# Kernel optimization log

Measured on AMD Instinct MI355X. Metric: run time of the kernel, lower is better.

Reference implementation:

```python
import jax, jax.numpy as jnp
import numpy as np

# GraphConvolutionSparse forward:
#   x = sparse_dropout(X)            (dropout=0.0 -> identity, kept faithful)
#   h = X @ W                        (sparse-dense matmul via segment_sum)
#   h = A @ h                        (sparse-dense matmul via segment_sum)
#   out = relu(h)

DROPOUT = 0.0  # layer default; keep_prob = 1 - dropout

def setup_inputs() -> dict:
    key = jax.random.key(0)
    k1, k2, k3, k4, k5, k6, k7 = jax.random.split(key, 7)
    N = 100000       # nodes
    D_IN = 512       # input feature dim
    D_OUT = 128      # output feature dim
    NNZ_X = 800000   # nonzeros in sparse feature matrix
    N_E = 1600000    # adjacency nonzeros (edges)
    x_vals = jax.random.normal(k1, (NNZ_X,), dtype=jnp.float32)
    x_rows = jax.random.randint(k2, (NNZ_X,), 0, N, dtype=jnp.int32)
    x_cols = jax.random.randint(k3, (NNZ_X,), 0, D_IN, dtype=jnp.int32)
    adj_vals = jax.random.uniform(k4, (N_E,), dtype=jnp.float32)
    adj_rows = jax.random.randint(k5, (N_E,), 0, N, dtype=jnp.int32)
    adj_cols = jax.random.randint(k6, (N_E,), 0, N, dtype=jnp.int32)
    init_range = np.sqrt(6.0 / (D_IN + D_OUT)).astype(np.float32)
    W = jax.random.uniform(k7, (D_IN, D_OUT), minval=-init_range, maxval=init_range, dtype=jnp.float32)
    return {"x_vals": x_vals, "x_rows": x_rows, "x_cols": x_cols,
            "adj_vals": adj_vals, "adj_rows": adj_rows, "adj_cols": adj_cols,
            "W": W, "n_nodes": N}

def reference(x_vals, x_rows, x_cols, adj_vals, adj_rows, adj_cols, W, n_nodes):
    keep_prob = 1.0 - DROPOUT
    # sparse dropout: with dropout=0.0 the mask keeps all entries and scale is 1,
    # so it reduces to the deterministic identity (faithful to tf semantics).
    vals = x_vals * (1.0 / keep_prob)
    # h = X @ W : gather weight rows by feature column, scale, scatter-add by node row
    xw = jax.ops.segment_sum(vals[:, None] * W[x_cols], x_rows, num_segments=n_nodes)  # [N, D_OUT]
    # out = A @ h : gather source-node rows, scale by edge weight, scatter-add to dest
    agg = jax.ops.segment_sum(adj_vals[:, None] * xw[adj_cols], adj_rows, num_segments=n_nodes)  # [N, D_OUT]
    return jax.nn.relu(agg)
```

## Files before the change

### kernel.cpp

```cpp
#include <hip/hip_runtime.h>
#include <hip/hip_fp16.h>


#define DOUT 128
#define RB 32
#define RB_BITS 5
#define NBMAX 4096
#define CAPL 1024
#define COLMASK 131071
#define CTH 128
#define CWAVES 2
#define CAPX 448
#define CAPA 768

static inline size_t align_up(size_t x, size_t a) { return (x + a - 1) & ~(a - 1); }

__device__ inline int2 nt_load_int2(const int2* p) {
    long long v = __builtin_nontemporal_load((const long long*)p);
    int2 r; r.x = (int)(unsigned int)(v & 0xffffffffLL); r.y = (int)(v >> 32);
    return r;
}
__device__ inline void nt_store_float2(float2* p, float2 v) {
    union { float2 f; long long l; } u; u.f = v;
    __builtin_nontemporal_store(u.l, (long long*)p);
}

__device__ inline int wave_incl_scan(int v, int lane) {
    #pragma unroll
    for (int off = 1; off < 64; off <<= 1) {
        int up = __shfl_up(v, off, 64);
        if (lane >= off) v += up;
    }
    return v;
}

__global__ __launch_bounds__(256) void prep_kernel(int* __restrict__ cnts, int ncnt,
                                                   const float* __restrict__ W,
                                                   __half2* __restrict__ Wh, int whtot) {
    int i = blockIdx.x * 256 + threadIdx.x;
    if (i < ncnt) cnts[i] = 0;
    if (i < whtot) {
        int c = i >> 6, l = i & 63;
        Wh[i] = __floats2half2_rn(W[(c << 7) + 2 * l], W[(c << 7) + 2 * l + 1]);
    }
}

__global__ __launch_bounds__(256) void hist_coarse(const int* __restrict__ xr, int nx,
                                                   const int* __restrict__ ar, int na,
                                                   int* __restrict__ cx, int* __restrict__ ca) {
    __shared__ int h[2 * NBMAX];
    for (int i = threadIdx.x; i < 2 * NBMAX; i += 256) h[i] = 0;
    __syncthreads();
    int base = blockIdx.x * 4096;
    int tot = nx + na;
    #pragma unroll
    for (int k = 0; k < 16; ++k) {
        int i = base + k * 256 + threadIdx.x;
        if (i < tot) {
            if (i < nx) atomicAdd(&h[xr[i] >> RB_BITS], 1);
            else        atomicAdd(&h[NBMAX + (ar[i - nx] >> RB_BITS)], 1);
        }
    }
    __syncthreads();
    for (int i = threadIdx.x; i < 2 * NBMAX; i += 256) {
        int c = h[i];
        if (c) {
            if (i < NBMAX) atomicAdd(&cx[i], c);
            else           atomicAdd(&ca[i - NBMAX], c);
        }
    }
}

__global__ __launch_bounds__(1024) void scan_nb(const int* __restrict__ cx, const int* __restrict__ ca,
                                                int* __restrict__ bx, int* __restrict__ ba,
                                                int* __restrict__ curx, int* __restrict__ cura, int nb) {
    const int* c = blockIdx.x ? ca : cx;
    int* bs  = blockIdx.x ? ba : bx;
    int* cur = blockIdx.x ? cura : curx;
    __shared__ int wsum[16];
    __shared__ int woff[16];
    __shared__ int carry_s, chunk_tot;
    int tid = threadIdx.x, lane = tid & 63, wid = tid >> 6;
    if (tid == 0) carry_s = 0;
    __syncthreads();
    for (int base = 0; base < nb; base += 1024) {
        int i = base + tid;
        int v = (i < nb) ? c[i] : 0;
        int incl = wave_incl_scan(v, lane);
        if (lane == 63) wsum[wid] = incl;
        __syncthreads();
        if (wid == 0 && lane < 16) {
            int s = wsum[lane];
            int is = s;
            #pragma unroll
            for (int off = 1; off < 16; off <<= 1) {
                int up = __shfl_up(is, off, 64);
                if (lane >= off) is += up;
            }
            woff[lane] = is - s;
            if (lane == 15) chunk_tot = is;
        }
        __syncthreads();
        int excl = incl - v + woff[wid] + carry_s;
        if (i < nb) { bs[i] = excl; cur[i] = excl; }
        __syncthreads();
        if (tid == 0) carry_s += chunk_tot;
        __syncthreads();
    }
    if (tid == 0) bs[nb] = carry_s;
}

__global__ __launch_bounds__(512) void bucket_scatter2(const int* __restrict__ xr, const int* __restrict__ xc,
                                                       const float* __restrict__ xv, int nx,
                                                       const int* __restrict__ ar, const int* __restrict__ ac,
                                                       const float* __restrict__ av, int na,
                                                       int* __restrict__ curx, int* __restrict__ cura,
                                                       int2* __restrict__ stx, int2* __restrict__ sta,
                                                       int nb, int nblk_x, int capx, int capa) {
    const int* rows; const int* cols; const float* vals; int n;
    int* gcur; int2* stage; int base; int cap;
    if (blockIdx.x < nblk_x) {
        rows = xr; cols = xc; vals = xv; n = nx; gcur = curx; stage = stx;
        base = blockIdx.x * 4096; cap = capx;
    } else {
        rows = ar; cols = ac; vals = av; n = na; gcur = cura; stage = sta;
        base = (blockIdx.x - nblk_x) * 4096; cap = capa;
    }
    __shared__ int h[NBMAX];
    __shared__ int bcur[NBMAX];
    for (int i = threadIdx.x; i < nb; i += 512) h[i] = 0;
    __syncthreads();
    int rr[8]; int cc[8]; float vv[8];
    #pragma unroll
    for (int k = 0; k < 8; ++k) {
        int i = base + k * 512 + threadIdx.x;
        rr[k] = -1;
        if (i < n) {
            rr[k] = __builtin_nontemporal_load(&rows[i]);
            cc[k] = __builtin_nontemporal_load(&cols[i]);
            vv[k] = __builtin_nontemporal_load(&vals[i]);
            atomicAdd(&h[rr[k] >> RB_BITS], 1);
        }
    }
    __syncthreads();
    for (int b = threadIdx.x; b < nb; b += 512) {
        int c = h[b];
        if (c) {
            int r = atomicAdd(&gcur[b], c);
            bcur[b] = (cap > 0) ? (b * cap + r) : r;
        }
    }
    __syncthreads();
    #pragma unroll
    for (int k = 0; k < 8; ++k) {
        if (rr[k] >= 0) {
            int b = rr[k] >> RB_BITS;
            int p = atomicAdd(&bcur[b], 1);
            if (cap == 0 || p < b * cap + cap)
                stage[p] = make_int2(((rr[k] & (RB - 1)) << 17) | cc[k], __float_as_int(vv[k]));
        }
    }
}


__global__ __launch_bounds__(CTH) void consumer_xw(const int* __restrict__ bx, const int* __restrict__ gcnt,
                                                   const int2* __restrict__ stage,
                                                   const __half2* __restrict__ Wh, __half2* __restrict__ xwh,
                                                   int N, int cap) {
    __shared__ int2 sp[CAPL];
    __shared__ int hoff[RB + 1];
    __shared__ int curs[RB];
    int b = blockIdx.x;
    int s, cnt;
    if (cap > 0) { s = b * cap; cnt = min(gcnt[b], cap); }
    else         { s = bx[b]; cnt = bx[b + 1] - s; }
    int tid = threadIdx.x, lane = tid & 63, wid = tid >> 6;
    bool fast = (cnt <= CAPL);
    if (tid < RB) curs[tid] = 0;
    __syncthreads();
    int2 pr[8];
    if (fast) {
        #pragma unroll
        for (int k = 0; k < 8; ++k) {
            int i = k * CTH + tid;
            if (i < cnt) {
                pr[k] = nt_load_int2(&stage[s + i]);
                atomicAdd(&curs[(pr[k].x >> 17) & (RB - 1)], 1);
            }
        }
    }
    __syncthreads();
    if (wid == 0) {
        int v = (lane < RB) ? curs[lane] : 0;
        int incl = wave_incl_scan(v, lane);
        if (lane < RB) {
            int excl = incl - v;
            hoff[lane] = excl;
            curs[lane] = excl;
            if (lane == RB - 1) hoff[RB] = incl;
        }
    }
    __syncthreads();
    if (fast) {
        #pragma unroll
        for (int k = 0; k < 8; ++k) {
            int i = k * CTH + tid;
            if (i < cnt) {
                int r = (pr[k].x >> 17) & (RB - 1);
                sp[atomicAdd(&curs[r], 1)] = pr[k];
            }
        }
    }
    __syncthreads();
    int row0 = b << RB_BITS;
    #pragma unroll 1
    for (int rr = 0; rr < RB / CWAVES; ++rr) {
        int r = wid + rr * CWAVES;
        int grow = row0 + r;
        if (grow >= N) continue;
        float ax = 0.f, ay = 0.f;
        if (fast) {
            int j = hoff[r], o1 = hoff[r + 1];
            for (; j + 3 < o1; j += 4) {
                int2 c0 = sp[j], c1 = sp[j + 1], c2 = sp[j + 2], c3 = sp[j + 3];
                float2 w0 = __half22float2(Wh[((size_t)(c0.x & COLMASK) << 6) + lane]);
                float2 w1 = __half22float2(Wh[((size_t)(c1.x & COLMASK) << 6) + lane]);
                float2 w2 = __half22float2(Wh[((size_t)(c2.x & COLMASK) << 6) + lane]);
                float2 w3 = __half22float2(Wh[((size_t)(c3.x & COLMASK) << 6) + lane]);
                float v0 = __int_as_float(c0.y), v1 = __int_as_float(c1.y);
                float v2 = __int_as_float(c2.y), v3 = __int_as_float(c3.y);
                ax += v0 * w0.x + v1 * w1.x + v2 * w2.x + v3 * w3.x;
                ay += v0 * w0.y + v1 * w1.y + v2 * w2.y + v3 * w3.y;
            }
            for (; j < o1; ++j) {
                int2 c0 = sp[j];
                float2 w0 = __half22float2(Wh[((size_t)(c0.x & COLMASK) << 6) + lane]);
                float v0 = __int_as_float(c0.y);
                ax += v0 * w0.x; ay += v0 * w0.y;
            }
        } else {
            for (int j = 0; j < cnt; ++j) {
                int2 c0 = stage[s + j];
                if (((c0.x >> 17) & (RB - 1)) == r) {
                    float2 w0 = __half22float2(Wh[((size_t)(c0.x & COLMASK) << 6) + lane]);
                    float v0 = __int_as_float(c0.y);
                    ax += v0 * w0.x; ay += v0 * w0.y;
                }
            }
        }
        xwh[((size_t)grow << 6) + lane] = __float22half2_rn(make_float2(ax, ay));
    }
}

__global__ __launch_bounds__(CTH) void consumer_adj(const int* __restrict__ ba, const int* __restrict__ gcnt,
                                                    const int2* __restrict__ stage,
                                                    const __half2* __restrict__ xwh, float* __restrict__ out,
                                                    int N, int cap) {
    __shared__ int2 sp[CAPL];
    __shared__ int hoff[RB + 1];
    __shared__ int curs[RB];
    int b = blockIdx.x;
    int s, cnt;
    if (cap > 0) { s = b * cap; cnt = min(gcnt[b], cap); }
    else         { s = ba[b]; cnt = ba[b + 1] - s; }
    int tid = threadIdx.x, lane = tid & 63, wid = tid >> 6;
    bool fast = (cnt <= CAPL);
    if (tid < RB) curs[tid] = 0;
    __syncthreads();
    int2 pr[8];
    if (fast) {
        #pragma unroll
        for (int k = 0; k < 8; ++k) {
            int i = k * CTH + tid;
            if (i < cnt) {
                pr[k] = nt_load_int2(&stage[s + i]);
                atomicAdd(&curs[(pr[k].x >> 17) & (RB - 1)], 1);
            }
        }
    }
    __syncthreads();
    if (wid == 0) {
        int v = (lane < RB) ? curs[lane] : 0;
        int incl = wave_incl_scan(v, lane);
        if (lane < RB) {
            int excl = incl - v;
            hoff[lane] = excl;
            curs[lane] = excl;
            if (lane == RB - 1) hoff[RB] = incl;
        }
    }
    __syncthreads();
    if (fast) {
        #pragma unroll
        for (int k = 0; k < 8; ++k) {
            int i = k * CTH + tid;
            if (i < cnt) {
                int r = (pr[k].x >> 17) & (RB - 1);
                sp[atomicAdd(&curs[r], 1)] = pr[k];
            }
        }
    }
    __syncthreads();
    int row0 = b << RB_BITS;
    #pragma unroll 1
    for (int rr = 0; rr < RB / CWAVES; ++rr) {
        int r = wid + rr * CWAVES;
        int grow = row0 + r;
        if (grow >= N) continue;
        float ax = 0.f, ay = 0.f;
        if (fast) {
            int j = hoff[r], o1 = hoff[r + 1];
            for (; j + 3 < o1; j += 4) {
                int2 c0 = sp[j], c1 = sp[j + 1], c2 = sp[j + 2], c3 = sp[j + 3];
                float2 h0 = __half22float2(xwh[((size_t)(c0.x & COLMASK) << 6) + lane]);
                float2 h1 = __half22float2(xwh[((size_t)(c1.x & COLMASK) << 6) + lane]);
                float2 h2 = __half22float2(xwh[((size_t)(c2.x & COLMASK) << 6) + lane]);
                float2 h3 = __half22float2(xwh[((size_t)(c3.x & COLMASK) << 6) + lane]);
                float v0 = __int_as_float(c0.y), v1 = __int_as_float(c1.y);
                float v2 = __int_as_float(c2.y), v3 = __int_as_float(c3.y);
                ax += v0 * h0.x + v1 * h1.x + v2 * h2.x + v3 * h3.x;
                ay += v0 * h0.y + v1 * h1.y + v2 * h2.y + v3 * h3.y;
            }
            for (; j < o1; ++j) {
                int2 c0 = sp[j];
                float2 h0 = __half22float2(xwh[((size_t)(c0.x & COLMASK) << 6) + lane]);
                float v0 = __int_as_float(c0.y);
                ax += v0 * h0.x; ay += v0 * h0.y;
            }
        } else {
            for (int j = 0; j < cnt; ++j) {
                int2 c0 = stage[s + j];
                if (((c0.x >> 17) & (RB - 1)) == r) {
                    float2 h0 = __half22float2(xwh[((size_t)(c0.x & COLMASK) << 6) + lane]);
                    float v0 = __int_as_float(c0.y);
                    ax += v0 * h0.x; ay += v0 * h0.y;
                }
            }
        }
        nt_store_float2(&((float2*)(out + (size_t)grow * DOUT))[lane],
                        make_float2(fmaxf(ax, 0.f), fmaxf(ay, 0.f)));
    }
}

__global__ void spmm_xw_atomic(const float* __restrict__ x_vals, const int* __restrict__ x_rows,
                               const int* __restrict__ x_cols, const float* __restrict__ W,
                               float* __restrict__ xw, int nnz) {
    long long t = (long long)blockIdx.x * blockDim.x + threadIdx.x;
    int i = (int)(t >> 7), d = (int)(t & 127);
    if (i >= nnz) return;
    atomicAdd(&xw[(long long)x_rows[i] * DOUT + d], x_vals[i] * W[(long long)x_cols[i] * DOUT + d]);
}
__global__ void spmm_adj_atomic(const float* __restrict__ adj_vals, const int* __restrict__ adj_rows,
                                const int* __restrict__ adj_cols, const float* __restrict__ xw,
                                float* __restrict__ out, int n_e) {
    long long t = (long long)blockIdx.x * blockDim.x + threadIdx.x;
    int e = (int)(t >> 7), d = (int)(t & 127);
    if (e >= n_e) return;
    atomicAdd(&out[(long long)adj_rows[e] * DOUT + d], adj_vals[e] * xw[(long long)adj_cols[e] * DOUT + d]);
}
__global__ void relu_kernel(float4* __restrict__ out, int n4) {
    int i = blockIdx.x * blockDim.x + threadIdx.x;
    if (i >= n4) return;
    float4 v = out[i];
    v.x = fmaxf(v.x, 0.f); v.y = fmaxf(v.y, 0.f);
    v.z = fmaxf(v.z, 0.f); v.w = fmaxf(v.w, 0.f);
    out[i] = v;
}

extern "C" void kernel_launch(void* const* d_in, const int* in_sizes, int n_in,
                              void* d_out, int out_size, void* d_ws, size_t ws_size,
                              hipStream_t stream) {
    const float* x_vals   = (const float*)d_in[0];
    const int*   x_rows   = (const int*)d_in[1];
    const int*   x_cols   = (const int*)d_in[2];
    const float* adj_vals = (const float*)d_in[3];
    const int*   adj_rows = (const int*)d_in[4];
    const int*   adj_cols = (const int*)d_in[5];
    const float* W        = (const float*)d_in[6];
    float* out = (float*)d_out;

    const int nnz_x = in_sizes[0];
    const int n_e   = in_sizes[3];
    const int N     = out_size / DOUT;
    const int D_IN  = in_sizes[6] / DOUT;
    const int nb    = (N + RB - 1) / RB;

    char* ws = (char*)d_ws;
    size_t off = 0;
    size_t xw_off   = off; off = align_up(off + (size_t)N * DOUT * sizeof(__half), 128);
    size_t wh_off   = off; off = align_up(off + (size_t)D_IN * 64 * sizeof(__half2), 128);
    size_t cx_off   = off; off += (size_t)NBMAX * sizeof(int);
    size_t ca_off   = off; off = align_up(off + (size_t)NBMAX * sizeof(int), 128);
    size_t bx_off   = off; off = align_up(off + (size_t)(NBMAX + 1) * sizeof(int), 128);
    size_t baoff    = off; off = align_up(off + (size_t)(NBMAX + 1) * sizeof(int), 128);
    size_t head = off;
    size_t sxc_off = head;
    size_t sac_off = align_up(sxc_off + (size_t)nb * CAPX * sizeof(int2), 128);
    size_t needed_cap = align_up(sac_off + (size_t)nb * CAPA * sizeof(int2), 128);
    size_t sxm_off = head;
    size_t sam_off = align_up(sxm_off + (size_t)nnz_x * sizeof(int2), 128);
    size_t needed_mid = align_up(sam_off + (size_t)n_e * sizeof(int2), 128);

    bool ok_dims = (nb <= NBMAX) && (N <= (COLMASK + 1));
    const int ncnt = 2 * NBMAX;
    const int whtot = D_IN * 64;
    const int prep_n = (ncnt > whtot ? ncnt : whtot);

    if (ok_dims && ws_size >= needed_cap) {
        __half2* xwh  = (__half2*)(ws + xw_off);
        __half2* Wh   = (__half2*)(ws + wh_off);
        int*  cx      = (int*)(ws + cx_off);
        int*  ca      = (int*)(ws + ca_off);
        int2* stage_x = (int2*)(ws + sxc_off);
        int2* stage_a = (int2*)(ws + sac_off);

        prep_kernel<<<(prep_n + 255) / 256, 256, 0, stream>>>(cx, ncnt, W, Wh, whtot);

        int nblk_x = (nnz_x + 4095) / 4096;
        int nblk_a = (n_e + 4095) / 4096;
        bucket_scatter2<<<nblk_x + nblk_a, 512, 0, stream>>>(x_rows, x_cols, x_vals, nnz_x,
                                                             adj_rows, adj_cols, adj_vals, n_e,
                                                             cx, ca, stage_x, stage_a,
                                                             nb, nblk_x, CAPX, CAPA);
        consumer_xw<<<nb, CTH, 0, stream>>>(nullptr, cx, stage_x, Wh, xwh, N, CAPX);
        consumer_adj<<<nb, CTH, 0, stream>>>(nullptr, ca, stage_a, xwh, out, N, CAPA);
    } else if (ok_dims && ws_size >= needed_mid) {
        __half2* xwh  = (__half2*)(ws + xw_off);
        __half2* Wh   = (__half2*)(ws + wh_off);
        int*  cx      = (int*)(ws + cx_off);
        int*  ca      = (int*)(ws + ca_off);
        int*  bx      = (int*)(ws + bx_off);
        int*  ba      = (int*)(ws + baoff);
        int2* stage_x = (int2*)(ws + sxm_off);
        int2* stage_a = (int2*)(ws + sam_off);

        prep_kernel<<<(prep_n + 255) / 256, 256, 0, stream>>>(cx, ncnt, W, Wh, whtot);

        int tot = nnz_x + n_e;
        hist_coarse<<<(tot + 4095) / 4096, 256, 0, stream>>>(x_rows, nnz_x, adj_rows, n_e, cx, ca);
        scan_nb<<<2, 1024, 0, stream>>>(cx, ca, bx, ba, cx, ca, nb);

        int nblk_x = (nnz_x + 4095) / 4096;
        int nblk_a = (n_e + 4095) / 4096;
        bucket_scatter2<<<nblk_x + nblk_a, 512, 0, stream>>>(x_rows, x_cols, x_vals, nnz_x,
                                                             adj_rows, adj_cols, adj_vals, n_e,
                                                             cx, ca, stage_x, stage_a,
                                                             nb, nblk_x, 0, 0);
        consumer_xw<<<nb, CTH, 0, stream>>>(bx, nullptr, stage_x, Wh, xwh, N, 0);
        consumer_adj<<<nb, CTH, 0, stream>>>(ba, nullptr, stage_a, xwh, out, N, 0);
    } else {
        float* xw = (float*)ws;
        hipMemsetAsync(xw, 0, (size_t)out_size * sizeof(float), stream);
        hipMemsetAsync(out, 0, (size_t)out_size * sizeof(float), stream);
        long long t1 = (long long)nnz_x * DOUT;
        spmm_xw_atomic<<<(int)((t1 + 255) / 256), 256, 0, stream>>>(x_vals, x_rows, x_cols, W, xw, nnz_x);
        long long t2 = (long long)n_e * DOUT;
        spmm_adj_atomic<<<(int)((t2 + 255) / 256), 256, 0, stream>>>(adj_vals, adj_rows, adj_cols, xw, out, n_e);
        relu_kernel<<<(out_size / 4 + 255) / 256, 256, 0, stream>>>((float4*)out, out_size / 4);
    }
}
```

Measured before the change: 220.5 us.

## Restructure adjacency consumer to sort edges by column chunk with LDS accumulators

The adjacency consumer now runs 256 threads (4 waves), with each wave owning 8 destination rows. Inside a bucket, edges are counting-sorted by a key that combines a source-column chunk with the row. Each wave walks the chunks in order and accumulates into a per-row float2 array in shared memory, then applies ReLU and stores. The goal is more waves per bucket and more local gathers from the half-precision xw table, at the cost of a shared-memory read-modify-write per edge and a 256-entry scan. Separately, the bucket scatter kernel now handles 8192 elements per block (16 per thread) instead of 4096, halving the block count and the global cursor atomics.

```diff
diff --git a/kernel.cpp b/kernel.cpp
--- a/kernel.cpp
+++ b/kernel.cpp
@@ -5,13 +5,18 @@
 #define DOUT 128
 #define RB 32
 #define RB_BITS 5
+#define NCH 8
+#define KMAXK 256
 #define NBMAX 4096
-#define CAPL 1024
+#define CAPLX 1024
 #define COLMASK 131071
-#define CTH 128
-#define CWAVES 2
+#define CTHX 128
+#define CWX 2
+#define CTHA 256
+#define CWA 4
 #define CAPX 448
 #define CAPA 768
+#define SCB 8192
 
 static inline size_t align_up(size_t x, size_t a) { return (x + a - 1) & ~(a - 1); }
 
@@ -121,18 +126,18 @@
     int* gcur; int2* stage; int base; int cap;
     if (blockIdx.x < nblk_x) {
         rows = xr; cols = xc; vals = xv; n = nx; gcur = curx; stage = stx;
-        base = blockIdx.x * 4096; cap = capx;
+        base = blockIdx.x * SCB; cap = capx;
     } else {
         rows = ar; cols = ac; vals = av; n = na; gcur = cura; stage = sta;
-        base = (blockIdx.x - nblk_x) * 4096; cap = capa;
+        base = (blockIdx.x - nblk_x) * SCB; cap = capa;
     }
     __shared__ int h[NBMAX];
     __shared__ int bcur[NBMAX];
     for (int i = threadIdx.x; i < nb; i += 512) h[i] = 0;
     __syncthreads();
-    int rr[8]; int cc[8]; float vv[8];
+    int rr[16]; int cc[16]; float vv[16];
     #pragma unroll
-    for (int k = 0; k < 8; ++k) {
+    for (int k = 0; k < 16; ++k) {
         int i = base + k * 512 + threadIdx.x;
         rr[k] = -1;
         if (i < n) {
@@ -152,7 +157,7 @@
     }
     __syncthreads();
     #pragma unroll
-    for (int k = 0; k < 8; ++k) {
+    for (int k = 0; k < 16; ++k) {
         if (rr[k] >= 0) {
             int b = rr[k] >> RB_BITS;
             int p = atomicAdd(&bcur[b], 1);
@@ -163,11 +168,11 @@
 }
 
 
-__global__ __launch_bounds__(CTH) void consumer_xw(const int* __restrict__ bx, const int* __restrict__ gcnt,
-                                                   const int2* __restrict__ stage,
-                                                   const __half2* __restrict__ Wh, __half2* __restrict__ xwh,
-                                                   int N, int cap) {
-    __shared__ int2 sp[CAPL];
+__global__ __launch_bounds__(CTHX) void consumer_xw(const int* __restrict__ bx, const int* __restrict__ gcnt,
+                                                    const int2* __restrict__ stage,
+                                                    const __half2* __restrict__ Wh, __half2* __restrict__ xwh,
+                                                    int N, int cap) {
+    __shared__ int2 sp[CAPLX];
     __shared__ int hoff[RB + 1];
     __shared__ int curs[RB];
     int b = blockIdx.x;
@@ -175,14 +180,14 @@
     if (cap > 0) { s = b * cap; cnt = min(gcnt[b], cap); }
     else         { s = bx[b]; cnt = bx[b + 1] - s; }
     int tid = threadIdx.x, lane = tid & 63, wid = tid >> 6;
-    bool fast = (cnt <= CAPL);
+    bool fast = (cnt <= CAPLX);
     if (tid < RB) curs[tid] = 0;
     __syncthreads();
     int2 pr[8];
     if (fast) {
         #pragma unroll
         for (int k = 0; k < 8; ++k) {
-            int i = k * CTH + tid;
+            int i = k * CTHX + tid;
             if (i < cnt) {
                 pr[k] = nt_load_int2(&stage[s + i]);
                 atomicAdd(&curs[(pr[k].x >> 17) & (RB - 1)], 1);
@@ -204,7 +209,7 @@
     if (fast) {
         #pragma unroll
         for (int k = 0; k < 8; ++k) {
-            int i = k * CTH + tid;
+            int i = k * CTHX + tid;
             if (i < cnt) {
                 int r = (pr[k].x >> 17) & (RB - 1);
                 sp[atomicAdd(&curs[r], 1)] = pr[k];
@@ -214,8 +219,8 @@
     __syncthreads();
     int row0 = b << RB_BITS;
     #pragma unroll 1
-    for (int rr = 0; rr < RB / CWAVES; ++rr) {
-        int r = wid + rr * CWAVES;
+    for (int rr = 0; rr < RB / CWX; ++rr) {
+        int r = wid + rr * CWX;
         int grow = row0 + r;
         if (grow >= N) continue;
         float ax = 0.f, ay = 0.f;
@@ -252,82 +257,112 @@
     }
 }
 
-__global__ __launch_bounds__(CTH) void consumer_adj(const int* __restrict__ ba, const int* __restrict__ gcnt,
-                                                    const int2* __restrict__ stage,
-                                                    const __half2* __restrict__ xwh, float* __restrict__ out,
-                                                    int N, int cap) {
-    __shared__ int2 sp[CAPL];
-    __shared__ int hoff[RB + 1];
-    __shared__ int curs[RB];
+
+__global__ __launch_bounds__(CTHA) void consumer_adj(const int* __restrict__ ba, const int* __restrict__ gcnt,
+                                                     const int2* __restrict__ stage,
+                                                     const __half2* __restrict__ xwh, float* __restrict__ out,
+                                                     int N, int cap) {
+    __shared__ int2 sp[CAPA];
+    __shared__ float2 accL[RB][64];
+    __shared__ int off[KMAXK + 1];
+    __shared__ int curs[KMAXK];
     int b = blockIdx.x;
     int s, cnt;
     if (cap > 0) { s = b * cap; cnt = min(gcnt[b], cap); }
     else         { s = ba[b]; cnt = ba[b + 1] - s; }
     int tid = threadIdx.x, lane = tid & 63, wid = tid >> 6;
-    bool fast = (cnt <= CAPL);
-    if (tid < RB) curs[tid] = 0;
-    __syncthreads();
-    int2 pr[8];
+    bool fast = (cnt <= CAPA);
+    curs[tid] = 0;
+    {
+        float2* af = &accL[0][0];
+        #pragma unroll
+        for (int k = 0; k < 8; ++k) af[tid + k * CTHA] = make_float2(0.f, 0.f);
+    }
+    __syncthreads();
+    int2 pr[3];
     if (fast) {
         #pragma unroll
-        for (int k = 0; k < 8; ++k) {
-            int i = k * CTH + tid;
+        for (int k = 0; k < 3; ++k) {
+            int i = k * CTHA + tid;
             if (i < cnt) {
                 pr[k] = nt_load_int2(&stage[s + i]);
-                atomicAdd(&curs[(pr[k].x >> 17) & (RB - 1)], 1);
+                int key = (((pr[k].x >> 14) & (NCH - 1)) << RB_BITS) | ((pr[k].x >> 17) & (RB - 1));
+                atomicAdd(&curs[key], 1);
             }
         }
     }
     __syncthreads();
     if (wid == 0) {
-        int v = (lane < RB) ? curs[lane] : 0;
-        int incl = wave_incl_scan(v, lane);
-        if (lane < RB) {
-            int excl = incl - v;
-            hoff[lane] = excl;
-            curs[lane] = excl;
-            if (lane == RB - 1) hoff[RB] = incl;
-        }
+        int carry = 0;
+        #pragma unroll
+        for (int q = 0; q < 4; ++q) {
+            int k = (q << 6) + lane;
+            int v = curs[k];
+            int incl = wave_incl_scan(v, lane) + carry;
+            off[k] = incl - v;
+            curs[k] = incl - v;
+            carry = __shfl(incl, 63, 64);
+        }
+        if (lane == 0) off[KMAXK] = carry;
     }
     __syncthreads();
     if (fast) {
         #pragma unroll
-        for (int k = 0; k < 8; ++k) {
-            int i = k * CTH + tid;
+        for (int k = 0; k < 3; ++k) {
+            int i = k * CTHA + tid;
             if (i < cnt) {
-                int r = (pr[k].x >> 17) & (RB - 1);
-                sp[atomicAdd(&curs[r], 1)] = pr[k];
+                int key = (((pr[k].x >> 14) & (NCH - 1)) << RB_BITS) | ((pr[k].x >> 17) & (RB - 1));
+                sp[atomicAdd(&curs[key], 1)] = pr[k];
             }
         }
     }
     __syncthreads();
     int row0 = b << RB_BITS;
-    #pragma unroll 1
-    for (int rr = 0; rr < RB / CWAVES; ++rr) {
-        int r = wid + rr * CWAVES;
-        int grow = row0 + r;
-        if (grow >= N) continue;
-        float ax = 0.f, ay = 0.f;
-        if (fast) {
-            int j = hoff[r], o1 = hoff[r + 1];
+    if (fast) {
+        int aw = wid << 3;
+        #pragma unroll 1
+        for (int ch = 0; ch < NCH; ++ch) {
+            int j  = off[(ch << RB_BITS) + aw];
+            int o1 = off[(ch << RB_BITS) + aw + 8];
             for (; j + 3 < o1; j += 4) {
                 int2 c0 = sp[j], c1 = sp[j + 1], c2 = sp[j + 2], c3 = sp[j + 3];
                 float2 h0 = __half22float2(xwh[((size_t)(c0.x & COLMASK) << 6) + lane]);
                 float2 h1 = __half22float2(xwh[((size_t)(c1.x & COLMASK) << 6) + lane]);
                 float2 h2 = __half22float2(xwh[((size_t)(c2.x & COLMASK) << 6) + lane]);
                 float2 h3 = __half22float2(xwh[((size_t)(c3.x & COLMASK) << 6) + lane]);
+                int r0 = (c0.x >> 17) & (RB - 1), r1 = (c1.x >> 17) & (RB - 1);
+                int r2 = (c2.x >> 17) & (RB - 1), r3 = (c3.x >> 17) & (RB - 1);
                 float v0 = __int_as_float(c0.y), v1 = __int_as_float(c1.y);
                 float v2 = __int_as_float(c2.y), v3 = __int_as_float(c3.y);
-                ax += v0 * h0.x + v1 * h1.x + v2 * h2.x + v3 * h3.x;
-                ay += v0 * h0.y + v1 * h1.y + v2 * h2.y + v3 * h3.y;
+                float2 a0 = accL[r0][lane]; a0.x += v0 * h0.x; a0.y += v0 * h0.y; accL[r0][lane] = a0;
+                float2 a1 = accL[r1][lane]; a1.x += v1 * h1.x; a1.y += v1 * h1.y; accL[r1][lane] = a1;
+                float2 a2 = accL[r2][lane]; a2.x += v2 * h2.x; a2.y += v2 * h2.y; accL[r2][lane] = a2;
+                float2 a3 = accL[r3][lane]; a3.x += v3 * h3.x; a3.y += v3 * h3.y; accL[r3][lane] = a3;
             }
             for (; j < o1; ++j) {
                 int2 c0 = sp[j];
                 float2 h0 = __half22float2(xwh[((size_t)(c0.x & COLMASK) << 6) + lane]);
+                int r0 = (c0.x >> 17) & (RB - 1);
                 float v0 = __int_as_float(c0.y);
-                ax += v0 * h0.x; ay += v0 * h0.y;
-            }
-        } else {
+                float2 a0 = accL[r0][lane]; a0.x += v0 * h0.x; a0.y += v0 * h0.y; accL[r0][lane] = a0;
+            }
+        }
+        #pragma unroll
+        for (int q = 0; q < 8; ++q) {
+            int grow = row0 + aw + q;
+            if (grow < N) {
+                float2 a = accL[aw + q][lane];
+                nt_store_float2(&((float2*)(out + (size_t)grow * DOUT))[lane],
+                                make_float2(fmaxf(a.x, 0.f), fmaxf(a.y, 0.f)));
+            }
+        }
+    } else {
+        #pragma unroll 1
+        for (int rr = 0; rr < RB / CWA; ++rr) {
+            int r = wid + rr * CWA;
+            int grow = row0 + r;
+            if (grow >= N) continue;
+            float ax = 0.f, ay = 0.f;
             for (int j = 0; j < cnt; ++j) {
                 int2 c0 = stage[s + j];
                 if (((c0.x >> 17) & (RB - 1)) == r) {
@@ -336,9 +371,9 @@
                     ax += v0 * h0.x; ay += v0 * h0.y;
                 }
             }
-        }
-        nt_store_float2(&((float2*)(out + (size_t)grow * DOUT))[lane],
-                        make_float2(fmaxf(ax, 0.f), fmaxf(ay, 0.f)));
+            nt_store_float2(&((float2*)(out + (size_t)grow * DOUT))[lane],
+                            make_float2(fmaxf(ax, 0.f), fmaxf(ay, 0.f)));
+        }
     }
 }
 
@@ -416,14 +451,14 @@
 
         prep_kernel<<<(prep_n + 255) / 256, 256, 0, stream>>>(cx, ncnt, W, Wh, whtot);
 
-        int nblk_x = (nnz_x + 4095) / 4096;
-        int nblk_a = (n_e + 4095) / 4096;
+        int nblk_x = (nnz_x + SCB - 1) / SCB;
+        int nblk_a = (n_e + SCB - 1) / SCB;
         bucket_scatter2<<<nblk_x + nblk_a, 512, 0, stream>>>(x_rows, x_cols, x_vals, nnz_x,
                                                              adj_rows, adj_cols, adj_vals, n_e,
                                                              cx, ca, stage_x, stage_a,
                                                              nb, nblk_x, CAPX, CAPA);
-        consumer_xw<<<nb, CTH, 0, stream>>>(nullptr, cx, stage_x, Wh, xwh, N, CAPX);
-        consumer_adj<<<nb, CTH, 0, stream>>>(nullptr, ca, stage_a, xwh, out, N, CAPA);
+        consumer_xw<<<nb, CTHX, 0, stream>>>(nullptr, cx, stage_x, Wh, xwh, N, CAPX);
+        consumer_adj<<<nb, CTHA, 0, stream>>>(nullptr, ca, stage_a, xwh, out, N, CAPA);
     } else if (ok_dims && ws_size >= needed_mid) {
         __half2* xwh  = (__half2*)(ws + xw_off);
         __half2* Wh   = (__half2*)(ws + wh_off);
@@ -440,14 +475,14 @@
         hist_coarse<<<(tot + 4095) / 4096, 256, 0, stream>>>(x_rows, nnz_x, adj_rows, n_e, cx, ca);
         scan_nb<<<2, 1024, 0, stream>>>(cx, ca, bx, ba, cx, ca, nb);
 
-        int nblk_x = (nnz_x + 4095) / 4096;
-        int nblk_a = (n_e + 4095) / 4096;
+        int nblk_x = (nnz_x + SCB - 1) / SCB;
+        int nblk_a = (n_e + SCB - 1) / SCB;
         bucket_scatter2<<<nblk_x + nblk_a, 512, 0, stream>>>(x_rows, x_cols, x_vals, nnz_x,
                                                              adj_rows, adj_cols, adj_vals, n_e,
                                                              cx, ca, stage_x, stage_a,
                                                              nb, nblk_x, 0, 0);
-        consumer_xw<<<nb, CTH, 0, stream>>>(bx, nullptr, stage_x, Wh, xwh, N, 0);
-        consumer_adj<<<nb, CTH, 0, stream>>>(ba, nullptr, stage_a, xwh, out, N, 0);
+        consumer_xw<<<nb, CTHX, 0, stream>>>(bx, nullptr, stage_x, Wh, xwh, N, 0);
+        consumer_adj<<<nb, CTHA, 0, stream>>>(ba, nullptr, stage_a, xwh, out, N, 0);
     } else {
         float* xw = (float*)ws;
         hipMemsetAsync(xw, 0, (size_t)out_size * sizeof(float), stream);
```

Result: no change. 223.3 us (+1.3%).
